# Performance work log

Hardware: AMD Instinct MI355X
Metric: run time of the kernel (lower is better)

## Reference

```python
import jax, jax.numpy as jnp
import numpy as np

B, N, K = 16, 2500, 16
NIN, NMED, WIN, WMED, NETYPE = 64, 64, 32, 32, 3


def _p(key, shape, scale=0.05):
    return jax.random.normal(key, shape, dtype=jnp.float32) * scale


def conv_bn_relu(x, W, b, scale, shift):
    # 1x1 Conv2d (NCHW) + eval-mode BatchNorm folded to affine (scale/shift) + ReLU
    y = jnp.einsum('oc,bcnk->bonk', W, x) + b[None, :, None, None]
    y = y * scale[None, :, None, None] + shift[None, :, None, None]
    return jax.nn.relu(y)


def mp_conv_v2(nf, wf, nn_idx, etype, theta, theta_b, gateW, gate_b, edgeW, edge_b):
    # nf: [B,Cn,N,1], wf: [B,Cw,N,K], nn_idx/etype: [B,N,K]
    n3 = nf[:, :, :, 0]                                   # [B,Cn,N]
    nb = jax.vmap(lambda f, idx: f[:, idx])(n3, nn_idx)   # gather -> [B,Cn,N,K]
    # per-edge-type linear transform of gathered neighbor features (small fixed loop over types)
    msg = jnp.zeros(nb.shape, nb.dtype)
    for t in range(theta.shape[0]):
        mask = (etype == t).astype(nb.dtype)[:, None]     # [B,1,N,K]
        m = jnp.einsum('oi,bink->bonk', theta[t], nb) + theta_b[t][None, :, None, None]
        msg = msg + mask * m
    # edge-feature gate on messages
    gate = jax.nn.sigmoid(jnp.einsum('oc,bcnk->bonk', gateW, wf) + gate_b[None, :, None, None])
    n_out = jax.nn.relu(jnp.mean(msg * gate, axis=3, keepdims=True))  # [B,Cn,N,1]
    # edge update from own feature + gathered neighbor feature
    cat = jnp.concatenate([wf, nb], axis=1)               # [B,Cw+Cn,N,K]
    w_out = jax.nn.relu(jnp.einsum('oc,bcnk->bonk', edgeW, cat) + edge_b[None, :, None, None])
    return n_out, w_out


def setup_inputs() -> dict:
    key = jax.random.key(0)
    ks = jax.random.split(key, 30)
    inp = {
        'node_feature': jax.random.normal(ks[0], (B, NIN, N, 1), jnp.float32),
        'weight_feature': jax.random.normal(ks[1], (B, WIN, N, K), jnp.float32),
        'etype': jax.random.randint(ks[2], (B, N, K), 0, NETYPE, dtype=jnp.int32),
        'nn_idx': jax.random.randint(ks[3], (B, N, K), 0, N, dtype=jnp.int32),
        # nconv1: nin->nmed (conv W,b + folded-BN scale,shift)
        'nW1': _p(ks[4], (NMED, NIN)), 'nb1': _p(ks[5], (NMED,)),
        'ns1': 1.0 + _p(ks[6], (NMED,)), 'nsh1': _p(ks[7], (NMED,)),
        'wW1': _p(ks[8], (WMED, WIN)), 'wb1': _p(ks[9], (WMED,)),
        'ws1': 1.0 + _p(ks[10], (WMED,)), 'wsh1': _p(ks[11], (WMED,)),
        # mp_conv_v2 params
        'theta': _p(ks[12], (NETYPE, NMED, NMED)), 'theta_b': _p(ks[13], (NETYPE, NMED)),
        'gateW': _p(ks[14], (NMED, WMED)), 'gate_b': _p(ks[15], (NMED,)),
        'edgeW': _p(ks[16], (WMED, WMED + NMED)), 'edge_b': _p(ks[17], (WMED,)),
        # nconv2: nmed->nin
        'nW2': _p(ks[18], (NIN, NMED)), 'nb2': _p(ks[19], (NIN,)),
        'ns2': 1.0 + _p(ks[20], (NIN,)), 'nsh2': _p(ks[21], (NIN,)),
        'wW2': _p(ks[22], (WIN, WMED)), 'wb2': _p(ks[23], (WIN,)),
        'ws2': 1.0 + _p(ks[24], (WIN,)), 'wsh2': _p(ks[25], (WIN,)),
    }
    return inp


def reference(node_feature, weight_feature, etype, nn_idx,
              nW1, nb1, ns1, nsh1, wW1, wb1, ws1, wsh1,
              theta, theta_b, gateW, gate_b, edgeW, edge_b,
              nW2, nb2, ns2, nsh2, wW2, wb2, ws2, wsh2):
    nf = conv_bn_relu(node_feature, nW1, nb1, ns1, nsh1)
    wf = conv_bn_relu(weight_feature, wW1, wb1, ws1, wsh1)
    nf, wf = mp_conv_v2(nf, wf, nn_idx, etype, theta, theta_b, gateW, gate_b, edgeW, edge_b)
    nf = conv_bn_relu(nf, nW2, nb2, ns2, nsh2)
    wf = conv_bn_relu(wf, wW2, wb2, ws2, wsh2)
    nf = nf + node_feature   # with_residual=True
    wf = wf + weight_feature
    return (nf, wf)
```

## Files before the change

kernel.cpp:

```cpp
#include <hip/hip_runtime.h>
#include <hip/hip_bf16.h>
#include <stdint.h>

#define B_ 16
#define N_ 2500

typedef unsigned short u16;
typedef __attribute__((ext_vector_type(8))) short bf16x8;
typedef __attribute__((ext_vector_type(4))) float f32x4;

__device__ __forceinline__ u16 f2bf_sw(float f) {
  unsigned u = __float_as_uint(f);
  return (u16)((u + 0x7fffu + ((u >> 16) & 1u)) >> 16);
}
__device__ __forceinline__ u16 f2bf(float f) {
  __hip_bfloat16 h = __float2bfloat16(f);
  return __builtin_bit_cast(u16, h);
}
__device__ __forceinline__ unsigned f2bf2(float lo, float hi) {
  return (unsigned)f2bf(lo) | ((unsigned)f2bf(hi) << 16);
}
__device__ __forceinline__ float sigm(float x) {
  return __builtin_amdgcn_rcpf(1.f + __expf(-x));
}

#define BLOB_U32 12448

__global__ __launch_bounds__(256) void k_pack(
    const float* __restrict__ theta, const float* __restrict__ edgeW,
    const float* __restrict__ gateW, const float* __restrict__ wW1,
    const float* __restrict__ wW2, const float* __restrict__ nW2,
    const float* __restrict__ theta_b, const float* __restrict__ gate_b,
    const float* __restrict__ edge_b,
    const float* __restrict__ ws1, const float* __restrict__ wb1, const float* __restrict__ wsh1,
    const float* __restrict__ ns2, const float* __restrict__ nb2, const float* __restrict__ nsh2,
    const float* __restrict__ ws2, const float* __restrict__ wb2, const float* __restrict__ wsh2,
    unsigned* __restrict__ blob) {
  const int tid = threadIdx.x;
  for (int q = tid; q < 6144; q += 256) {
    int f = q >> 8, lane = (q >> 2) & 63, jp = q & 3;
    int t = f >> 3, mt = (f >> 1) & 3, h = f & 1;
    int el = lane & 15, kg = lane >> 4;
    const float* s = theta + ((size_t)t * 64 + mt * 16 + el) * 64 + h * 32 + kg * 8 + jp * 2;
    blob[q] = (unsigned)f2bf_sw(s[0]) | ((unsigned)f2bf_sw(s[1]) << 16);
  }
  for (int q = tid; q < 1536; q += 256) {
    int f = q >> 8, lane = (q >> 2) & 63, jp = q & 3;
    int mt = f / 3, ss = f - mt * 3;
    int el = lane & 15, kg = lane >> 4;
    const float* s = edgeW + ((size_t)mt * 16 + el) * 96 + ss * 32 + kg * 8 + jp * 2;
    blob[6144 + q] = (unsigned)f2bf_sw(s[0]) | ((unsigned)f2bf_sw(s[1]) << 16);
  }
  for (int q = tid; q < 1024; q += 256) {
    int f = q >> 8, lane = (q >> 2) & 63, jp = q & 3;
    int el = lane & 15, kg = lane >> 4;
    const float* s = gateW + ((size_t)f * 16 + el) * 32 + kg * 8 + jp * 2;
    blob[7680 + q] = (unsigned)f2bf_sw(s[0]) | ((unsigned)f2bf_sw(s[1]) << 16);
  }
  for (int q = tid; q < 512; q += 256) {
    int f = q >> 8, lane = (q >> 2) & 63, jp = q & 3;
    int el = lane & 15, kg = lane >> 4;
    const float* s1 = wW1 + (size_t)(f * 16 + el) * 32 + kg * 8 + jp * 2;
    const float* s2 = wW2 + (size_t)(f * 16 + el) * 32 + kg * 8 + jp * 2;
    blob[8704 + q] = (unsigned)f2bf_sw(s1[0]) | ((unsigned)f2bf_sw(s1[1]) << 16);
    blob[9216 + q] = (unsigned)f2bf_sw(s2[0]) | ((unsigned)f2bf_sw(s2[1]) << 16);
  }
  for (int q = tid; q < 2048; q += 256) {
    int f = q >> 8, lane = (q >> 2) & 63, jp = q & 3;
    int mt = f >> 1, h = f & 1;
    int el = lane & 15, kg = lane >> 4;
    const float* s = nW2 + (size_t)(mt * 16 + el) * 64 + h * 32 + kg * 8 + jp * 2;
    blob[9728 + q] = (unsigned)f2bf_sw(s[0]) | ((unsigned)f2bf_sw(s[1]) << 16);
  }
  float* bf = (float*)blob;
  for (int i = tid; i < 672; i += 256) {
    float v;
    if (i < 192)      v = theta_b[i];
    else if (i < 256) v = gate_b[i - 192];
    else if (i < 320) v = ns2[i - 256];
    else if (i < 384) v = nb2[i - 320];
    else if (i < 448) v = nsh2[i - 384];
    else if (i < 480) v = edge_b[i - 448];
    else if (i < 512) v = ws1[i - 480];
    else if (i < 544) v = wb1[i - 512];
    else if (i < 576) v = wsh1[i - 544];
    else if (i < 608) v = ws2[i - 576];
    else if (i < 640) v = wb2[i - 608];
    else              v = wsh2[i - 640];
    bf[11776 + i] = v;
  }
}

__global__ __launch_bounds__(256) void k_nf1(
    const float* __restrict__ node, const float* __restrict__ W,
    const float* __restrict__ bia, const float* __restrict__ sc,
    const float* __restrict__ sh, u16* __restrict__ nf1b) {
  __shared__ __align__(16) u16 W_p[8 * 64 * 8];
  __shared__ float bia_s[64], sc_s[64], sh_s[64];
  const int tid = threadIdx.x;
  for (int q = tid; q < 2048; q += 256) {
    int f = q >> 8, lane = (q >> 2) & 63, jp = q & 3;
    int mt = f >> 1, h = f & 1;
    int fel = lane & 15, fkg = lane >> 4;
    const float* src = W + (size_t)(mt * 16 + fel) * 64 + h * 32 + fkg * 8 + jp * 2;
    ((unsigned*)W_p)[q] = f2bf2(src[0], src[1]);
  }
  if (tid < 64) { bia_s[tid] = bia[tid]; sc_s[tid] = sc[tid]; sh_s[tid] = sh[tid]; }
  __syncthreads();

  const int l = tid & 63, wv = tid >> 6;
  const int el = l & 15, kg = l >> 4;
  const int bn = blockIdx.x * 64 + wv * 16 + el;
  const int b = bn / N_;
  const int n = bn - b * N_;

  union UF { bf16x8 v; uint4 q; } xb0, xb1;
  const float* xp0 = node + (size_t)(b * 64 + kg * 8) * N_ + n;
  const float* xp1 = node + (size_t)(b * 64 + 32 + kg * 8) * N_ + n;
  {
    float a0[8], a1[8];
#pragma unroll
    for (int j = 0; j < 8; ++j) { a0[j] = xp0[(size_t)j * N_]; a1[j] = xp1[(size_t)j * N_]; }
    xb0.q.x = f2bf2(a0[0], a0[1]); xb0.q.y = f2bf2(a0[2], a0[3]);
    xb0.q.z = f2bf2(a0[4], a0[5]); xb0.q.w = f2bf2(a0[6], a0[7]);
    xb1.q.x = f2bf2(a1[0], a1[1]); xb1.q.y = f2bf2(a1[2], a1[3]);
    xb1.q.z = f2bf2(a1[4], a1[5]); xb1.q.w = f2bf2(a1[6], a1[7]);
  }
  const f32x4 z4 = {0.f, 0.f, 0.f, 0.f};
#pragma unroll
  for (int mt = 0; mt < 4; ++mt) {
    bf16x8 a0 = *(const bf16x8*)&W_p[((mt * 2 + 0) * 64 + l) * 8];
    bf16x8 a1 = *(const bf16x8*)&W_p[((mt * 2 + 1) * 64 + l) * 8];
    f32x4 acc = __builtin_amdgcn_mfma_f32_16x16x32_bf16(a0, xb0.v, z4, 0, 0, 0);
    acc = __builtin_amdgcn_mfma_f32_16x16x32_bf16(a1, xb1.v, acc, 0, 0, 0);
    int ob = mt * 16 + kg * 4;
    float4 s4 = *(const float4*)&sc_s[ob];
    float4 b4 = *(const float4*)&bia_s[ob];
    float4 h4 = *(const float4*)&sh_s[ob];
    uint2 d;
    d.x = f2bf2(fmaxf(fmaf(s4.x, acc[0] + b4.x, h4.x), 0.f),
                fmaxf(fmaf(s4.y, acc[1] + b4.y, h4.y), 0.f));
    d.y = f2bf2(fmaxf(fmaf(s4.z, acc[2] + b4.z, h4.z), 0.f),
                fmaxf(fmaf(s4.w, acc[3] + b4.w, h4.w), 0.f));
    *(uint2*)&nf1b[(size_t)bn * 64 + ob] = d;
  }
}

__global__ __launch_bounds__(512, 2) void k_fused(
    const float* __restrict__ node, const float* __restrict__ wfeat,
    const int* __restrict__ etype, const int* __restrict__ nn_idx,
    const u16* __restrict__ nf1b, const unsigned* __restrict__ blob,
    float* __restrict__ out_nf, float* __restrict__ out_wf) {

  __shared__ __align__(16) unsigned char sm[BLOB_U32 * 4];
  __shared__ __align__(16) u16 nout_bf[32 * 64];
  __shared__ __align__(16) u16 Rx[8][512];

  const int tid = threadIdx.x;
  for (int i = tid; i < BLOB_U32 / 4; i += 512)
    ((uint4*)sm)[i] = ((const uint4*)blob)[i];

  const u16* th_p   = (const u16*)sm;
  const u16* eW_p   = (const u16*)(sm + 24576);
  const u16* gW_p   = (const u16*)(sm + 30720);
  const u16* w1_p   = (const u16*)(sm + 34816);
  const u16* w2_p   = (const u16*)(sm + 36864);
  const u16* nW2f_p = (const u16*)(sm + 38912);
  const float* par = (const float*)(sm + 47104);
  const float* tb_s  = par;
  const float* gb_s  = par + 192;
  const float* ns2_s = par + 256;
  const float* nb2_s = par + 320;
  const float* nsh2_s= par + 384;
  const float* eb_s  = par + 448;
  const float* ws1_s = par + 480;
  const float* wb1_s = par + 512;
  const float* wsh1_s= par + 544;
  const float* ws2_s = par + 576;
  const float* wb2_s = par + 608;
  const float* wsh2_s= par + 640;

  const int pb = blockIdx.x;
  const int xcd = pb & 7, sub = pb >> 3;
  const int lb = (xcd < 2) ? (xcd * 157 + sub) : (2 * 157 + (xcd - 2) * 156 + sub);
  const int nbase = lb * 32;

  const int l = tid & 63, wv = tid >> 6;
  const int el = l & 15, kg = l >> 4;
  u16* const Rn = &Rx[wv][0];

  __syncthreads();

  const f32x4 z4 = {0.f, 0.f, 0.f, 0.f};

  int idxv[4], etv[4];
  bf16x8 nb0v[4], nb1v[4];
  union UF { bf16x8 v; uint4 q; } xv[4];

  idxv[0] = nn_idx[(nbase + wv) * 16 + el];
  etv[0]  = etype[(nbase + wv) * 16 + el];
  idxv[1] = nn_idx[(nbase + 8 + wv) * 16 + el];
  etv[1]  = etype[(nbase + 8 + wv) * 16 + el];
  {
    const int nid = nbase + wv;
    const int b = nid / N_, n = nid - b * N_;
    const u16* nbp = nf1b + ((size_t)b * N_ + idxv[0]) * 64 + kg * 8;
    nb0v[0] = *(const bf16x8*)nbp;
    nb1v[0] = *(const bf16x8*)(nbp + 32);
    const float* xp = wfeat + ((size_t)(b * 32 + kg * 8) * N_ + n) * 16 + el;
    float a[8];
#pragma unroll
    for (int j = 0; j < 8; ++j) a[j] = xp[(size_t)j * N_ * 16];
    xv[0].q.x = f2bf2(a[0], a[1]); xv[0].q.y = f2bf2(a[2], a[3]);
    xv[0].q.z = f2bf2(a[4], a[5]); xv[0].q.w = f2bf2(a[6], a[7]);
  }

#pragma unroll
  for (int it = 0; it < 4; ++it) {
    const int nid = nbase + it * 8 + wv;
    const int b = nid / N_;
    const int n = nid - b * N_;
    const int nl = it * 8 + wv;
    const int et = etv[it];

    if (it + 2 < 4) {
      idxv[it + 2] = nn_idx[(nbase + (it + 2) * 8 + wv) * 16 + el];
      etv[it + 2]  = etype[(nbase + (it + 2) * 8 + wv) * 16 + el];
    }
    if (it + 1 < 4) {
      const int nid2 = nbase + (it + 1) * 8 + wv;
      const int b2 = nid2 / N_, n2 = nid2 - b2 * N_;
      const u16* nbp = nf1b + ((size_t)b2 * N_ + idxv[it + 1]) * 64 + kg * 8;
      nb0v[it + 1] = *(const bf16x8*)nbp;
      nb1v[it + 1] = *(const bf16x8*)(nbp + 32);
      const float* xp = wfeat + ((size_t)(b2 * 32 + kg * 8) * N_ + n2) * 16 + el;
      float a[8];
#pragma unroll
      for (int j = 0; j < 8; ++j) a[j] = xp[(size_t)j * N_ * 16];
      xv[it + 1].q.x = f2bf2(a[0], a[1]); xv[it + 1].q.y = f2bf2(a[2], a[3]);
      xv[it + 1].q.z = f2bf2(a[4], a[5]); xv[it + 1].q.w = f2bf2(a[6], a[7]);
    }

#pragma unroll
    for (int mt = 0; mt < 2; ++mt) {
      bf16x8 a = *(const bf16x8*)&w1_p[(mt * 64 + l) * 8];
      f32x4 wc = __builtin_amdgcn_mfma_f32_16x16x32_bf16(a, xv[it].v, z4, 0, 0, 0);
      int ob = mt * 16 + kg * 4;
      float4 s4 = *(const float4*)&ws1_s[ob];
      float4 b4 = *(const float4*)&wb1_s[ob];
      float4 h4 = *(const float4*)&wsh1_s[ob];
      uint2 d;
      d.x = f2bf2(fmaxf(fmaf(s4.x, wc[0] + b4.x, h4.x), 0.f),
                  fmaxf(fmaf(s4.y, wc[1] + b4.y, h4.y), 0.f));
      d.y = f2bf2(fmaxf(fmaf(s4.z, wc[2] + b4.z, h4.z), 0.f),
                  fmaxf(fmaf(s4.w, wc[3] + b4.w, h4.w), 0.f));
      *(uint2*)&Rn[((mt * 2 + (kg >> 1)) * 16 + el) * 8 + (kg & 1) * 4] = d;
    }
    bf16x8 wff = *(const bf16x8*)&Rn[l * 8];

    f32x4 macc[4] = {z4, z4, z4, z4};
    {
      union { bf16x8 v; uint4 q; } nb0u, nb1u;
      nb0u.v = nb0v[it]; nb1u.v = nb1v[it];
#pragma unroll
      for (int t = 0; t < 3; ++t) {
        unsigned msk = (et == t) ? 0xffffffffu : 0u;
        union { bf16x8 v; uint4 q; } b0, b1;
        b0.q.x = nb0u.q.x & msk; b0.q.y = nb0u.q.y & msk;
        b0.q.z = nb0u.q.z & msk; b0.q.w = nb0u.q.w & msk;
        b1.q.x = nb1u.q.x & msk; b1.q.y = nb1u.q.y & msk;
        b1.q.z = nb1u.q.z & msk; b1.q.w = nb1u.q.w & msk;
#pragma unroll
        for (int mt = 0; mt < 4; ++mt) {
          bf16x8 a0 = *(const bf16x8*)&th_p[((t * 8 + mt * 2 + 0) * 64 + l) * 8];
          bf16x8 a1 = *(const bf16x8*)&th_p[((t * 8 + mt * 2 + 1) * 64 + l) * 8];
          macc[mt] = __builtin_amdgcn_mfma_f32_16x16x32_bf16(a0, b0.v, macc[mt], 0, 0, 0);
          macc[mt] = __builtin_amdgcn_mfma_f32_16x16x32_bf16(a1, b1.v, macc[mt], 0, 0, 0);
        }
      }
    }

    f32x4 eacc[2];
#pragma unroll
    for (int mt = 0; mt < 2; ++mt) {
      bf16x8 a0 = *(const bf16x8*)&eW_p[((mt * 3 + 0) * 64 + l) * 8];
      bf16x8 a1 = *(const bf16x8*)&eW_p[((mt * 3 + 1) * 64 + l) * 8];
      bf16x8 a2 = *(const bf16x8*)&eW_p[((mt * 3 + 2) * 64 + l) * 8];
      f32x4 acc = __builtin_amdgcn_mfma_f32_16x16x32_bf16(a0, wff, z4, 0, 0, 0);
      acc = __builtin_amdgcn_mfma_f32_16x16x32_bf16(a1, nb0v[it], acc, 0, 0, 0);
      acc = __builtin_amdgcn_mfma_f32_16x16x32_bf16(a2, nb1v[it], acc, 0, 0, 0);
      eacc[mt] = acc;
    }

    float p[16];
#pragma unroll
    for (int mt = 0; mt < 4; ++mt) {
      bf16x8 ga = *(const bf16x8*)&gW_p[(mt * 64 + l) * 8];
      f32x4 g = __builtin_amdgcn_mfma_f32_16x16x32_bf16(ga, wff, z4, 0, 0, 0);
      int ob = mt * 16 + kg * 4;
      float4 tb = *(const float4*)&tb_s[et * 64 + ob];
      float4 gb = *(const float4*)&gb_s[ob];
      p[mt * 4 + 0] = (macc[mt][0] + tb.x) * sigm(g[0] + gb.x);
      p[mt * 4 + 1] = (macc[mt][1] + tb.y) * sigm(g[1] + gb.y);
      p[mt * 4 + 2] = (macc[mt][2] + tb.z) * sigm(g[2] + gb.z);
      p[mt * 4 + 3] = (macc[mt][3] + tb.w) * sigm(g[3] + gb.w);
    }

    {
      const int b0 = el & 1, b1 = (el >> 1) & 1, b2 = (el >> 2) & 1, b3 = (el >> 3) & 1;
      float w8[8];
#pragma unroll
      for (int j = 0; j < 8; ++j) {
        float send = b0 ? p[2 * j] : p[2 * j + 1];
        float keep = b0 ? p[2 * j + 1] : p[2 * j];
        w8[j] = keep + __shfl_xor(send, 1);
      }
      float w4[4];
#pragma unroll
      for (int j = 0; j < 4; ++j) {
        float send = b1 ? w8[2 * j] : w8[2 * j + 1];
        float keep = b1 ? w8[2 * j + 1] : w8[2 * j];
        w4[j] = keep + __shfl_xor(send, 2);
      }
      float w2[2];
#pragma unroll
      for (int j = 0; j < 2; ++j) {
        float send = b2 ? w4[2 * j] : w4[2 * j + 1];
        float keep = b2 ? w4[2 * j + 1] : w4[2 * j];
        w2[j] = keep + __shfl_xor(send, 4);
      }
      float send = b3 ? w2[0] : w2[1];
      float keep = b3 ? w2[1] : w2[0];
      float z = keep + __shfl_xor(send, 8);
      float no = fmaxf(z * 0.0625f, 0.f);
      int ch = ((el >> 2) << 4) + (kg << 2) + (el & 3);
      int su = (ch >> 3) ^ (nl & 7);
      nout_bf[nl * 64 + su * 8 + (ch & 7)] = f2bf(no);
    }

#pragma unroll
    for (int mt = 0; mt < 2; ++mt) {
      int ob = mt * 16 + kg * 4;
      float4 eb4 = *(const float4*)&eb_s[ob];
      uint2 d;
      d.x = f2bf2(fmaxf(eacc[mt][0] + eb4.x, 0.f), fmaxf(eacc[mt][1] + eb4.y, 0.f));
      d.y = f2bf2(fmaxf(eacc[mt][2] + eb4.z, 0.f), fmaxf(eacc[mt][3] + eb4.w, 0.f));
      *(uint2*)&Rn[((mt * 2 + (kg >> 1)) * 16 + el) * 8 + (kg & 1) * 4] = d;
    }
    bf16x8 wof = *(const bf16x8*)&Rn[l * 8];

#pragma unroll
    for (int mt = 0; mt < 2; ++mt) {
      bf16x8 a = *(const bf16x8*)&w2_p[(mt * 64 + l) * 8];
      f32x4 fc = __builtin_amdgcn_mfma_f32_16x16x32_bf16(a, wof, z4, 0, 0, 0);
      int ob = mt * 16 + kg * 4;
      float4 s4 = *(const float4*)&ws2_s[ob];
      float4 b4 = *(const float4*)&wb2_s[ob];
      float4 h4 = *(const float4*)&wsh2_s[ob];
      float sv[4] = {s4.x, s4.y, s4.z, s4.w};
      float bv[4] = {b4.x, b4.y, b4.z, b4.w};
      float hv[4] = {h4.x, h4.y, h4.z, h4.w};
#pragma unroll
      for (int r = 0; r < 4; ++r) {
        int a2 = ((b * 32 + ob + r) * N_ + n) * 16 + el;
        float y = fmaxf(fmaf(sv[r], fc[r] + bv[r], hv[r]), 0.f);
        out_wf[a2] = y + wfeat[a2];
      }
    }
  }
  __syncthreads();

  {
    const int mt = wv & 3, ng = wv >> 2;
    const int node_l = ng * 16 + el;
    const int nid2 = nbase + node_l;
    const int b2 = nid2 / N_;
    const int n2 = nid2 - b2 * N_;
    const int sw = node_l & 7;
    bf16x8 nb0 = *(const bf16x8*)&nout_bf[node_l * 64 + ((0 + kg) ^ sw) * 8];
    bf16x8 nb1 = *(const bf16x8*)&nout_bf[node_l * 64 + ((4 + kg) ^ sw) * 8];
    bf16x8 a0 = *(const bf16x8*)&nW2f_p[((mt * 2 + 0) * 64 + l) * 8];
    bf16x8 a1 = *(const bf16x8*)&nW2f_p[((mt * 2 + 1) * 64 + l) * 8];
    f32x4 acc = __builtin_amdgcn_mfma_f32_16x16x32_bf16(a0, nb0, z4, 0, 0, 0);
    acc = __builtin_amdgcn_mfma_f32_16x16x32_bf16(a1, nb1, acc, 0, 0, 0);
#pragma unroll
    for (int i = 0; i < 4; ++i) {
      int ch = mt * 16 + kg * 4 + i;
      int off = (b2 * 64 + ch) * N_ + n2;
      float y = fmaxf(fmaf(ns2_s[ch], acc[i] + nb2_s[ch], nsh2_s[ch]), 0.f);
      out_nf[off] = y + node[off];
    }
  }
}

extern "C" void kernel_launch(void* const* d_in, const int* in_sizes, int n_in,
                              void* d_out, int out_size, void* d_ws, size_t ws_size,
                              hipStream_t stream) {
  const float* node    = (const float*)d_in[0];
  const float* wfeat   = (const float*)d_in[1];
  const int*   etype   = (const int*)d_in[2];
  const int*   nn_idx  = (const int*)d_in[3];
  const float* nW1     = (const float*)d_in[4];
  const float* nb1     = (const float*)d_in[5];
  const float* ns1     = (const float*)d_in[6];
  const float* nsh1    = (const float*)d_in[7];
  const float* wW1     = (const float*)d_in[8];
  const float* wb1     = (const float*)d_in[9];
  const float* ws1     = (const float*)d_in[10];
  const float* wsh1    = (const float*)d_in[11];
  const float* theta   = (const float*)d_in[12];
  const float* theta_b = (const float*)d_in[13];
  const float* gateW   = (const float*)d_in[14];
  const float* gate_b  = (const float*)d_in[15];
  const float* edgeW   = (const float*)d_in[16];
  const float* edge_b  = (const float*)d_in[17];
  const float* nW2     = (const float*)d_in[18];
  const float* nb2     = (const float*)d_in[19];
  const float* ns2     = (const float*)d_in[20];
  const float* nsh2    = (const float*)d_in[21];
  const float* wW2     = (const float*)d_in[22];
  const float* wb2     = (const float*)d_in[23];
  const float* ws2     = (const float*)d_in[24];
  const float* wsh2    = (const float*)d_in[25];

  u16*      nf1b = (u16*)d_ws;
  unsigned* blob = (unsigned*)((char*)d_ws + 5120000);
  float* out_nf = (float*)d_out;
  float* out_wf = (float*)d_out + (size_t)B_ * 64 * N_;

  k_pack<<<1, 256, 0, stream>>>(theta, edgeW, gateW, wW1, wW2, nW2,
                                theta_b, gate_b, edge_b,
                                ws1, wb1, wsh1, ns2, nb2, nsh2, ws2, wb2, wsh2,
                                blob);
  k_nf1<<<625, 256, 0, stream>>>(node, nW1, nb1, ns1, nsh1, nf1b);
  k_fused<<<1250, 512, 0, stream>>>(node, wfeat, etype, nn_idx, nf1b, blob,
                                    out_nf, out_wf);
}
```

Measured before the change: 129.3 us.

## Switch fused edge kernel from 16x16x32 to 32x32x16 MFMA tiles

Repacks all weight fragments in the pack kernel for the 32x32x16 bf16 MFMA layout and restructures the fused kernel so each wave handles two nodes (32 edges) per iteration over two iterations instead of one node over four. This cuts the MFMA instruction count, reuses each weight operand across more columns, and halves the loop trip count. In exchange it uses larger f32x16 accumulators, which raises register pressure under the 512-thread, 2-block launch bound, and doubles the per-wave LDS staging buffer. The mean reduction shuffle tree is extended to 32 values per lane.

```diff
diff --git a/kernel.cpp b/kernel.cpp
--- a/kernel.cpp
+++ b/kernel.cpp
@@ -8,6 +8,7 @@
 typedef unsigned short u16;
 typedef __attribute__((ext_vector_type(8))) short bf16x8;
 typedef __attribute__((ext_vector_type(4))) float f32x4;
+typedef __attribute__((ext_vector_type(16))) float f32x16;
 
 __device__ __forceinline__ u16 f2bf_sw(float f) {
   unsigned u = __float_as_uint(f);
@@ -39,29 +40,29 @@
   const int tid = threadIdx.x;
   for (int q = tid; q < 6144; q += 256) {
     int f = q >> 8, lane = (q >> 2) & 63, jp = q & 3;
-    int t = f >> 3, mt = (f >> 1) & 3, h = f & 1;
-    int el = lane & 15, kg = lane >> 4;
-    const float* s = theta + ((size_t)t * 64 + mt * 16 + el) * 64 + h * 32 + kg * 8 + jp * 2;
-    blob[q] = (unsigned)f2bf_sw(s[0]) | ((unsigned)f2bf_sw(s[1]) << 16);
+    int t = f >> 3, mt = (f >> 2) & 1, s = f & 3;
+    int m = lane & 31, hf = lane >> 5;
+    const float* src = theta + ((size_t)t * 64 + mt * 32 + m) * 64 + s * 16 + hf * 8 + jp * 2;
+    blob[q] = (unsigned)f2bf_sw(src[0]) | ((unsigned)f2bf_sw(src[1]) << 16);
   }
   for (int q = tid; q < 1536; q += 256) {
     int f = q >> 8, lane = (q >> 2) & 63, jp = q & 3;
-    int mt = f / 3, ss = f - mt * 3;
-    int el = lane & 15, kg = lane >> 4;
-    const float* s = edgeW + ((size_t)mt * 16 + el) * 96 + ss * 32 + kg * 8 + jp * 2;
-    blob[6144 + q] = (unsigned)f2bf_sw(s[0]) | ((unsigned)f2bf_sw(s[1]) << 16);
+    int m = lane & 31, hf = lane >> 5;
+    const float* src = edgeW + (size_t)m * 96 + f * 16 + hf * 8 + jp * 2;
+    blob[6144 + q] = (unsigned)f2bf_sw(src[0]) | ((unsigned)f2bf_sw(src[1]) << 16);
   }
   for (int q = tid; q < 1024; q += 256) {
     int f = q >> 8, lane = (q >> 2) & 63, jp = q & 3;
-    int el = lane & 15, kg = lane >> 4;
-    const float* s = gateW + ((size_t)f * 16 + el) * 32 + kg * 8 + jp * 2;
-    blob[7680 + q] = (unsigned)f2bf_sw(s[0]) | ((unsigned)f2bf_sw(s[1]) << 16);
+    int mt = f >> 1, s = f & 1;
+    int m = lane & 31, hf = lane >> 5;
+    const float* src = gateW + ((size_t)mt * 32 + m) * 32 + s * 16 + hf * 8 + jp * 2;
+    blob[7680 + q] = (unsigned)f2bf_sw(src[0]) | ((unsigned)f2bf_sw(src[1]) << 16);
   }
   for (int q = tid; q < 512; q += 256) {
     int f = q >> 8, lane = (q >> 2) & 63, jp = q & 3;
-    int el = lane & 15, kg = lane >> 4;
-    const float* s1 = wW1 + (size_t)(f * 16 + el) * 32 + kg * 8 + jp * 2;
-    const float* s2 = wW2 + (size_t)(f * 16 + el) * 32 + kg * 8 + jp * 2;
+    int m = lane & 31, hf = lane >> 5;
+    const float* s1 = wW1 + (size_t)m * 32 + f * 16 + hf * 8 + jp * 2;
+    const float* s2 = wW2 + (size_t)m * 32 + f * 16 + hf * 8 + jp * 2;
     blob[8704 + q] = (unsigned)f2bf_sw(s1[0]) | ((unsigned)f2bf_sw(s1[1]) << 16);
     blob[9216 + q] = (unsigned)f2bf_sw(s2[0]) | ((unsigned)f2bf_sw(s2[1]) << 16);
   }
@@ -154,7 +155,7 @@
 
   __shared__ __align__(16) unsigned char sm[BLOB_U32 * 4];
   __shared__ __align__(16) u16 nout_bf[32 * 64];
-  __shared__ __align__(16) u16 Rx[8][512];
+  __shared__ __align__(16) u16 Rx[8][1024];
 
   const int tid = threadIdx.x;
   for (int i = tid; i < BLOB_U32 / 4; i += 512)
@@ -186,197 +187,239 @@
   const int nbase = lb * 32;
 
   const int l = tid & 63, wv = tid >> 6;
-  const int el = l & 15, kg = l >> 4;
-  u16* const Rn = &Rx[wv][0];
+  const int col = l & 31, half = l >> 5;
+  const int en = col & 15, nd = col >> 4;
+  u16* const Rw = &Rx[wv][0];
 
   __syncthreads();
 
-  const f32x4 z4 = {0.f, 0.f, 0.f, 0.f};
-
-  int idxv[4], etv[4];
-  bf16x8 nb0v[4], nb1v[4];
-  union UF { bf16x8 v; uint4 q; } xv[4];
-
-  idxv[0] = nn_idx[(nbase + wv) * 16 + el];
-  etv[0]  = etype[(nbase + wv) * 16 + el];
-  idxv[1] = nn_idx[(nbase + 8 + wv) * 16 + el];
-  etv[1]  = etype[(nbase + 8 + wv) * 16 + el];
+  const f32x16 z16 = {0.f,0.f,0.f,0.f,0.f,0.f,0.f,0.f,0.f,0.f,0.f,0.f,0.f,0.f,0.f,0.f};
+
+  int idxv[2], etv[2];
+  bf16x8 nbf[2][4];
+  bf16x8 xf[2][2];
+
+  idxv[0] = nn_idx[(nbase + 2 * wv + nd) * 16 + en];
+  etv[0]  = etype[(nbase + 2 * wv + nd) * 16 + en];
+  idxv[1] = nn_idx[(nbase + 16 + 2 * wv + nd) * 16 + en];
+  etv[1]  = etype[(nbase + 16 + 2 * wv + nd) * 16 + en];
   {
-    const int nid = nbase + wv;
+    const int nid = nbase + 2 * wv + nd;
     const int b = nid / N_, n = nid - b * N_;
-    const u16* nbp = nf1b + ((size_t)b * N_ + idxv[0]) * 64 + kg * 8;
-    nb0v[0] = *(const bf16x8*)nbp;
-    nb1v[0] = *(const bf16x8*)(nbp + 32);
-    const float* xp = wfeat + ((size_t)(b * 32 + kg * 8) * N_ + n) * 16 + el;
-    float a[8];
-#pragma unroll
-    for (int j = 0; j < 8; ++j) a[j] = xp[(size_t)j * N_ * 16];
-    xv[0].q.x = f2bf2(a[0], a[1]); xv[0].q.y = f2bf2(a[2], a[3]);
-    xv[0].q.z = f2bf2(a[4], a[5]); xv[0].q.w = f2bf2(a[6], a[7]);
-  }
-
-#pragma unroll
-  for (int it = 0; it < 4; ++it) {
-    const int nid = nbase + it * 8 + wv;
+    const u16* nbp = nf1b + ((size_t)b * N_ + idxv[0]) * 64 + half * 8;
+#pragma unroll
+    for (int s = 0; s < 4; ++s) nbf[0][s] = *(const bf16x8*)(nbp + s * 16);
+    const float* xpp = wfeat + ((size_t)(b * 32 + half * 8) * N_ + n) * 16 + en;
+#pragma unroll
+    for (int s = 0; s < 2; ++s) {
+      float a[8];
+#pragma unroll
+      for (int j = 0; j < 8; ++j) a[j] = xpp[(size_t)(s * 16 + j) * N_ * 16];
+      union { bf16x8 v; uint4 q; } u;
+      u.q.x = f2bf2(a[0], a[1]); u.q.y = f2bf2(a[2], a[3]);
+      u.q.z = f2bf2(a[4], a[5]); u.q.w = f2bf2(a[6], a[7]);
+      xf[0][s] = u.v;
+    }
+  }
+
+#pragma unroll
+  for (int it = 0; it < 2; ++it) {
+    const int nid = nbase + it * 16 + 2 * wv + nd;
     const int b = nid / N_;
     const int n = nid - b * N_;
-    const int nl = it * 8 + wv;
+    const int nl = it * 16 + 2 * wv + nd;
     const int et = etv[it];
 
-    if (it + 2 < 4) {
-      idxv[it + 2] = nn_idx[(nbase + (it + 2) * 8 + wv) * 16 + el];
-      etv[it + 2]  = etype[(nbase + (it + 2) * 8 + wv) * 16 + el];
-    }
-    if (it + 1 < 4) {
-      const int nid2 = nbase + (it + 1) * 8 + wv;
+    if (it == 0) {
+      const int nid2 = nbase + 16 + 2 * wv + nd;
       const int b2 = nid2 / N_, n2 = nid2 - b2 * N_;
-      const u16* nbp = nf1b + ((size_t)b2 * N_ + idxv[it + 1]) * 64 + kg * 8;
-      nb0v[it + 1] = *(const bf16x8*)nbp;
-      nb1v[it + 1] = *(const bf16x8*)(nbp + 32);
-      const float* xp = wfeat + ((size_t)(b2 * 32 + kg * 8) * N_ + n2) * 16 + el;
-      float a[8];
-#pragma unroll
-      for (int j = 0; j < 8; ++j) a[j] = xp[(size_t)j * N_ * 16];
-      xv[it + 1].q.x = f2bf2(a[0], a[1]); xv[it + 1].q.y = f2bf2(a[2], a[3]);
-      xv[it + 1].q.z = f2bf2(a[4], a[5]); xv[it + 1].q.w = f2bf2(a[6], a[7]);
-    }
-
+      const u16* nbp = nf1b + ((size_t)b2 * N_ + idxv[1]) * 64 + half * 8;
+#pragma unroll
+      for (int s = 0; s < 4; ++s) nbf[1][s] = *(const bf16x8*)(nbp + s * 16);
+      const float* xpp = wfeat + ((size_t)(b2 * 32 + half * 8) * N_ + n2) * 16 + en;
+#pragma unroll
+      for (int s = 0; s < 2; ++s) {
+        float a[8];
+#pragma unroll
+        for (int j = 0; j < 8; ++j) a[j] = xpp[(size_t)(s * 16 + j) * N_ * 16];
+        union { bf16x8 v; uint4 q; } u;
+        u.q.x = f2bf2(a[0], a[1]); u.q.y = f2bf2(a[2], a[3]);
+        u.q.z = f2bf2(a[4], a[5]); u.q.w = f2bf2(a[6], a[7]);
+        xf[1][s] = u.v;
+      }
+    }
+
+    f32x16 wc;
+    {
+      bf16x8 a0 = *(const bf16x8*)&w1_p[(0 * 64 + l) * 8];
+      bf16x8 a1 = *(const bf16x8*)&w1_p[(1 * 64 + l) * 8];
+      wc = __builtin_amdgcn_mfma_f32_32x32x16_bf16(a0, xf[it][0], z16, 0, 0, 0);
+      wc = __builtin_amdgcn_mfma_f32_32x32x16_bf16(a1, xf[it][1], wc, 0, 0, 0);
+    }
+#pragma unroll
+    for (int q = 0; q < 4; ++q) {
+      int chb = q * 8 + 4 * half;
+      float4 s4 = *(const float4*)&ws1_s[chb];
+      float4 b4 = *(const float4*)&wb1_s[chb];
+      float4 h4 = *(const float4*)&wsh1_s[chb];
+      float y0 = fmaxf(fmaf(s4.x, wc[q * 4 + 0] + b4.x, h4.x), 0.f);
+      float y1 = fmaxf(fmaf(s4.y, wc[q * 4 + 1] + b4.y, h4.y), 0.f);
+      float y2 = fmaxf(fmaf(s4.z, wc[q * 4 + 2] + b4.z, h4.z), 0.f);
+      float y3 = fmaxf(fmaf(s4.w, wc[q * 4 + 3] + b4.w, h4.w), 0.f);
+      uint2 d; d.x = f2bf2(y0, y1); d.y = f2bf2(y2, y3);
+      int Q = 2 * q + half;
+      *(uint2*)&Rw[(Q >> 2) * 512 + (col + 32 * ((Q >> 1) & 1)) * 8 + (Q & 1) * 4] = d;
+    }
+    bf16x8 wff0 = *(const bf16x8*)&Rw[l * 8];
+    bf16x8 wff1 = *(const bf16x8*)&Rw[512 + l * 8];
+
+    f32x16 eacc;
+    {
+      bf16x8 e0 = *(const bf16x8*)&eW_p[(0 * 64 + l) * 8];
+      bf16x8 e1 = *(const bf16x8*)&eW_p[(1 * 64 + l) * 8];
+      bf16x8 e2 = *(const bf16x8*)&eW_p[(2 * 64 + l) * 8];
+      bf16x8 e3 = *(const bf16x8*)&eW_p[(3 * 64 + l) * 8];
+      bf16x8 e4 = *(const bf16x8*)&eW_p[(4 * 64 + l) * 8];
+      bf16x8 e5 = *(const bf16x8*)&eW_p[(5 * 64 + l) * 8];
+      eacc = __builtin_amdgcn_mfma_f32_32x32x16_bf16(e0, wff0, z16, 0, 0, 0);
+      eacc = __builtin_amdgcn_mfma_f32_32x32x16_bf16(e1, wff1, eacc, 0, 0, 0);
+      eacc = __builtin_amdgcn_mfma_f32_32x32x16_bf16(e2, nbf[it][0], eacc, 0, 0, 0);
+      eacc = __builtin_amdgcn_mfma_f32_32x32x16_bf16(e3, nbf[it][1], eacc, 0, 0, 0);
+      eacc = __builtin_amdgcn_mfma_f32_32x32x16_bf16(e4, nbf[it][2], eacc, 0, 0, 0);
+      eacc = __builtin_amdgcn_mfma_f32_32x32x16_bf16(e5, nbf[it][3], eacc, 0, 0, 0);
+    }
+#pragma unroll
+    for (int q = 0; q < 4; ++q) {
+      int chb = q * 8 + 4 * half;
+      float4 eb4 = *(const float4*)&eb_s[chb];
+      float y0 = fmaxf(eacc[q * 4 + 0] + eb4.x, 0.f);
+      float y1 = fmaxf(eacc[q * 4 + 1] + eb4.y, 0.f);
+      float y2 = fmaxf(eacc[q * 4 + 2] + eb4.z, 0.f);
+      float y3 = fmaxf(eacc[q * 4 + 3] + eb4.w, 0.f);
+      uint2 d; d.x = f2bf2(y0, y1); d.y = f2bf2(y2, y3);
+      int Q = 2 * q + half;
+      *(uint2*)&Rw[(Q >> 2) * 512 + (col + 32 * ((Q >> 1) & 1)) * 8 + (Q & 1) * 4] = d;
+    }
+    bf16x8 wof0 = *(const bf16x8*)&Rw[l * 8];
+    bf16x8 wof1 = *(const bf16x8*)&Rw[512 + l * 8];
+
+    f32x16 macc0 = z16, macc1 = z16;
+#pragma unroll
+    for (int t = 0; t < 3; ++t) {
+      unsigned msk = (et == t) ? 0xffffffffu : 0u;
+      bf16x8 bm[4];
+#pragma unroll
+      for (int s = 0; s < 4; ++s) {
+        union { bf16x8 v; uint4 q; } u;
+        u.v = nbf[it][s];
+        u.q.x &= msk; u.q.y &= msk; u.q.z &= msk; u.q.w &= msk;
+        bm[s] = u.v;
+      }
+#pragma unroll
+      for (int s = 0; s < 4; ++s) {
+        bf16x8 a0 = *(const bf16x8*)&th_p[((t * 8 + 0 * 4 + s) * 64 + l) * 8];
+        bf16x8 a1 = *(const bf16x8*)&th_p[((t * 8 + 1 * 4 + s) * 64 + l) * 8];
+        macc0 = __builtin_amdgcn_mfma_f32_32x32x16_bf16(a0, bm[s], macc0, 0, 0, 0);
+        macc1 = __builtin_amdgcn_mfma_f32_32x32x16_bf16(a1, bm[s], macc1, 0, 0, 0);
+      }
+    }
+
+    float p[32];
 #pragma unroll
     for (int mt = 0; mt < 2; ++mt) {
-      bf16x8 a = *(const bf16x8*)&w1_p[(mt * 64 + l) * 8];
-      f32x4 wc = __builtin_amdgcn_mfma_f32_16x16x32_bf16(a, xv[it].v, z4, 0, 0, 0);
-      int ob = mt * 16 + kg * 4;
-      float4 s4 = *(const float4*)&ws1_s[ob];
-      float4 b4 = *(const float4*)&wb1_s[ob];
-      float4 h4 = *(const float4*)&wsh1_s[ob];
-      uint2 d;
-      d.x = f2bf2(fmaxf(fmaf(s4.x, wc[0] + b4.x, h4.x), 0.f),
-                  fmaxf(fmaf(s4.y, wc[1] + b4.y, h4.y), 0.f));
-      d.y = f2bf2(fmaxf(fmaf(s4.z, wc[2] + b4.z, h4.z), 0.f),
-                  fmaxf(fmaf(s4.w, wc[3] + b4.w, h4.w), 0.f));
-      *(uint2*)&Rn[((mt * 2 + (kg >> 1)) * 16 + el) * 8 + (kg & 1) * 4] = d;
-    }
-    bf16x8 wff = *(const bf16x8*)&Rn[l * 8];
-
-    f32x4 macc[4] = {z4, z4, z4, z4};
+      bf16x8 g0 = *(const bf16x8*)&gW_p[((mt * 2 + 0) * 64 + l) * 8];
+      bf16x8 g1 = *(const bf16x8*)&gW_p[((mt * 2 + 1) * 64 + l) * 8];
+      f32x16 gacc = __builtin_amdgcn_mfma_f32_32x32x16_bf16(g0, wff0, z16, 0, 0, 0);
+      gacc = __builtin_amdgcn_mfma_f32_32x32x16_bf16(g1, wff1, gacc, 0, 0, 0);
+#pragma unroll
+      for (int q = 0; q < 4; ++q) {
+        int chb = mt * 32 + q * 8 + 4 * half;
+        float4 tb4 = *(const float4*)&tb_s[et * 64 + chb];
+        float4 gb4 = *(const float4*)&gb_s[chb];
+        float mv0 = (mt ? macc1[q * 4 + 0] : macc0[q * 4 + 0]) + tb4.x;
+        float mv1 = (mt ? macc1[q * 4 + 1] : macc0[q * 4 + 1]) + tb4.y;
+        float mv2 = (mt ? macc1[q * 4 + 2] : macc0[q * 4 + 2]) + tb4.z;
+        float mv3 = (mt ? macc1[q * 4 + 3] : macc0[q * 4 + 3]) + tb4.w;
+        p[mt * 16 + q * 4 + 0] = mv0 * sigm(gacc[q * 4 + 0] + gb4.x);
+        p[mt * 16 + q * 4 + 1] = mv1 * sigm(gacc[q * 4 + 1] + gb4.y);
+        p[mt * 16 + q * 4 + 2] = mv2 * sigm(gacc[q * 4 + 2] + gb4.z);
+        p[mt * 16 + q * 4 + 3] = mv3 * sigm(gacc[q * 4 + 3] + gb4.w);
+      }
+    }
+
     {
-      union { bf16x8 v; uint4 q; } nb0u, nb1u;
-      nb0u.v = nb0v[it]; nb1u.v = nb1v[it];
-#pragma unroll
-      for (int t = 0; t < 3; ++t) {
-        unsigned msk = (et == t) ? 0xffffffffu : 0u;
-        union { bf16x8 v; uint4 q; } b0, b1;
-        b0.q.x = nb0u.q.x & msk; b0.q.y = nb0u.q.y & msk;
-        b0.q.z = nb0u.q.z & msk; b0.q.w = nb0u.q.w & msk;
-        b1.q.x = nb1u.q.x & msk; b1.q.y = nb1u.q.y & msk;
-        b1.q.z = nb1u.q.z & msk; b1.q.w = nb1u.q.w & msk;
-#pragma unroll
-        for (int mt = 0; mt < 4; ++mt) {
-          bf16x8 a0 = *(const bf16x8*)&th_p[((t * 8 + mt * 2 + 0) * 64 + l) * 8];
-          bf16x8 a1 = *(const bf16x8*)&th_p[((t * 8 + mt * 2 + 1) * 64 + l) * 8];
-          macc[mt] = __builtin_amdgcn_mfma_f32_16x16x32_bf16(a0, b0.v, macc[mt], 0, 0, 0);
-          macc[mt] = __builtin_amdgcn_mfma_f32_16x16x32_bf16(a1, b1.v, macc[mt], 0, 0, 0);
-        }
-      }
-    }
-
-    f32x4 eacc[2];
-#pragma unroll
-    for (int mt = 0; mt < 2; ++mt) {
-      bf16x8 a0 = *(const bf16x8*)&eW_p[((mt * 3 + 0) * 64 + l) * 8];
-      bf16x8 a1 = *(const bf16x8*)&eW_p[((mt * 3 + 1) * 64 + l) * 8];
-      bf16x8 a2 = *(const bf16x8*)&eW_p[((mt * 3 + 2) * 64 + l) * 8];
-      f32x4 acc = __builtin_amdgcn_mfma_f32_16x16x32_bf16(a0, wff, z4, 0, 0, 0);
-      acc = __builtin_amdgcn_mfma_f32_16x16x32_bf16(a1, nb0v[it], acc, 0, 0, 0);
-      acc = __builtin_amdgcn_mfma_f32_16x16x32_bf16(a2, nb1v[it], acc, 0, 0, 0);
-      eacc[mt] = acc;
-    }
-
-    float p[16];
-#pragma unroll
-    for (int mt = 0; mt < 4; ++mt) {
-      bf16x8 ga = *(const bf16x8*)&gW_p[(mt * 64 + l) * 8];
-      f32x4 g = __builtin_amdgcn_mfma_f32_16x16x32_bf16(ga, wff, z4, 0, 0, 0);
-      int ob = mt * 16 + kg * 4;
-      float4 tb = *(const float4*)&tb_s[et * 64 + ob];
-      float4 gb = *(const float4*)&gb_s[ob];
-      p[mt * 4 + 0] = (macc[mt][0] + tb.x) * sigm(g[0] + gb.x);
-      p[mt * 4 + 1] = (macc[mt][1] + tb.y) * sigm(g[1] + gb.y);
-      p[mt * 4 + 2] = (macc[mt][2] + tb.z) * sigm(g[2] + gb.z);
-      p[mt * 4 + 3] = (macc[mt][3] + tb.w) * sigm(g[3] + gb.w);
-    }
-
-    {
-      const int b0 = el & 1, b1 = (el >> 1) & 1, b2 = (el >> 2) & 1, b3 = (el >> 3) & 1;
-      float w8[8];
-#pragma unroll
-      for (int j = 0; j < 8; ++j) {
+      const int b0 = en & 1, b1 = (en >> 1) & 1, b2 = (en >> 2) & 1, b3 = (en >> 3) & 1;
+      float r16[16];
+#pragma unroll
+      for (int j = 0; j < 16; ++j) {
         float send = b0 ? p[2 * j] : p[2 * j + 1];
         float keep = b0 ? p[2 * j + 1] : p[2 * j];
-        w8[j] = keep + __shfl_xor(send, 1);
-      }
-      float w4[4];
+        r16[j] = keep + __shfl_xor(send, 1);
+      }
+      float r8[8];
+#pragma unroll
+      for (int j = 0; j < 8; ++j) {
+        float send = b1 ? r16[2 * j] : r16[2 * j + 1];
+        float keep = b1 ? r16[2 * j + 1] : r16[2 * j];
+        r8[j] = keep + __shfl_xor(send, 2);
+      }
+      float r4[4];
 #pragma unroll
       for (int j = 0; j < 4; ++j) {
-        float send = b1 ? w8[2 * j] : w8[2 * j + 1];
-        float keep = b1 ? w8[2 * j + 1] : w8[2 * j];
-        w4[j] = keep + __shfl_xor(send, 2);
-      }
-      float w2[2];
+        float send = b2 ? r8[2 * j] : r8[2 * j + 1];
+        float keep = b2 ? r8[2 * j + 1] : r8[2 * j];
+        r4[j] = keep + __shfl_xor(send, 4);
+      }
+      float r2[2];
 #pragma unroll
       for (int j = 0; j < 2; ++j) {
-        float send = b2 ? w4[2 * j] : w4[2 * j + 1];
-        float keep = b2 ? w4[2 * j + 1] : w4[2 * j];
-        w2[j] = keep + __shfl_xor(send, 4);
-      }
-      float send = b3 ? w2[0] : w2[1];
-      float keep = b3 ? w2[1] : w2[0];
-      float z = keep + __shfl_xor(send, 8);
-      float no = fmaxf(z * 0.0625f, 0.f);
-      int ch = ((el >> 2) << 4) + (kg << 2) + (el & 3);
-      int su = (ch >> 3) ^ (nl & 7);
-      nout_bf[nl * 64 + su * 8 + (ch & 7)] = f2bf(no);
-    }
-
-#pragma unroll
-    for (int mt = 0; mt < 2; ++mt) {
-      int ob = mt * 16 + kg * 4;
-      float4 eb4 = *(const float4*)&eb_s[ob];
-      uint2 d;
-      d.x = f2bf2(fmaxf(eacc[mt][0] + eb4.x, 0.f), fmaxf(eacc[mt][1] + eb4.y, 0.f));
-      d.y = f2bf2(fmaxf(eacc[mt][2] + eb4.z, 0.f), fmaxf(eacc[mt][3] + eb4.w, 0.f));
-      *(uint2*)&Rn[((mt * 2 + (kg >> 1)) * 16 + el) * 8 + (kg & 1) * 4] = d;
-    }
-    bf16x8 wof = *(const bf16x8*)&Rn[l * 8];
-
-#pragma unroll
-    for (int mt = 0; mt < 2; ++mt) {
-      bf16x8 a = *(const bf16x8*)&w2_p[(mt * 64 + l) * 8];
-      f32x4 fc = __builtin_amdgcn_mfma_f32_16x16x32_bf16(a, wof, z4, 0, 0, 0);
-      int ob = mt * 16 + kg * 4;
-      float4 s4 = *(const float4*)&ws2_s[ob];
-      float4 b4 = *(const float4*)&wb2_s[ob];
-      float4 h4 = *(const float4*)&wsh2_s[ob];
-      float sv[4] = {s4.x, s4.y, s4.z, s4.w};
-      float bv[4] = {b4.x, b4.y, b4.z, b4.w};
-      float hv[4] = {h4.x, h4.y, h4.z, h4.w};
-#pragma unroll
-      for (int r = 0; r < 4; ++r) {
-        int a2 = ((b * 32 + ob + r) * N_ + n) * 16 + el;
-        float y = fmaxf(fmaf(sv[r], fc[r] + bv[r], hv[r]), 0.f);
-        out_wf[a2] = y + wfeat[a2];
+        float send = b3 ? r4[2 * j] : r4[2 * j + 1];
+        float keep = b3 ? r4[2 * j + 1] : r4[2 * j];
+        r2[j] = keep + __shfl_xor(send, 8);
+      }
+      int ch0 = (en & 3) + 8 * ((en >> 2) & 3) + 4 * half;
+      float v0 = fmaxf(r2[0] * 0.0625f, 0.f);
+      float v1 = fmaxf(r2[1] * 0.0625f, 0.f);
+      nout_bf[nl * 64 + (((ch0 >> 3) ^ (nl & 7)) << 3) + (ch0 & 7)] = f2bf(v0);
+      int ch1 = ch0 + 32;
+      nout_bf[nl * 64 + (((ch1 >> 3) ^ (nl & 7)) << 3) + (ch1 & 7)] = f2bf(v1);
+    }
+
+    {
+      bf16x8 a0 = *(const bf16x8*)&w2_p[(0 * 64 + l) * 8];
+      bf16x8 a1 = *(const bf16x8*)&w2_p[(1 * 64 + l) * 8];
+      f32x16 fc = __builtin_amdgcn_mfma_f32_32x32x16_bf16(a0, wof0, z16, 0, 0, 0);
+      fc = __builtin_amdgcn_mfma_f32_32x32x16_bf16(a1, wof1, fc, 0, 0, 0);
+#pragma unroll
+      for (int q = 0; q < 4; ++q) {
+        int chb = q * 8 + 4 * half;
+        float4 s4 = *(const float4*)&ws2_s[chb];
+        float4 b4 = *(const float4*)&wb2_s[chb];
+        float4 h4 = *(const float4*)&wsh2_s[chb];
+        float sv[4] = {s4.x, s4.y, s4.z, s4.w};
+        float bv[4] = {b4.x, b4.y, b4.z, b4.w};
+        float hv[4] = {h4.x, h4.y, h4.z, h4.w};
+#pragma unroll
+        for (int i = 0; i < 4; ++i) {
+          int ch = chb + i;
+          size_t a2 = (((size_t)b * 32 + ch) * N_ + n) * 16 + en;
+          float y = fmaxf(fmaf(sv[i], fc[q * 4 + i] + bv[i], hv[i]), 0.f);
+          out_wf[a2] = y + wfeat[a2];
+        }
       }
     }
   }
   __syncthreads();
 
   {
+    const int el = l & 15, kg = l >> 4;
     const int mt = wv & 3, ng = wv >> 2;
     const int node_l = ng * 16 + el;
     const int nid2 = nbase + node_l;
     const int b2 = nid2 / N_;
     const int n2 = nid2 - b2 * N_;
     const int sw = node_l & 7;
+    const f32x4 z4 = {0.f, 0.f, 0.f, 0.f};
     bf16x8 nb0 = *(const bf16x8*)&nout_bf[node_l * 64 + ((0 + kg) ^ sw) * 8];
     bf16x8 nb1 = *(const bf16x8*)&nout_bf[node_l * 64 + ((4 + kg) ^ sw) * 8];
     bf16x8 a0 = *(const bf16x8*)&nW2f_p[((mt * 2 + 0) * 64 + l) * 8];
@@ -386,7 +429,7 @@
 #pragma unroll
     for (int i = 0; i < 4; ++i) {
       int ch = mt * 16 + kg * 4 + i;
-      int off = (b2 * 64 + ch) * N_ + n2;
+      size_t off = ((size_t)b2 * 64 + ch) * N_ + n2;
       float y = fmaxf(fmaf(ns2_s[ch], acc[i] + nb2_s[ch], nsh2_s[ch]), 0.f);
       out_nf[off] = y + node[off];
     }
```

New measurement: 132.8 us. +2.7%, slower.

## Drop software prefetch pipeline and raise occupancy to four blocks per CU

Applied to the files above, without the earlier changes.

Removes the register-held prefetch of neighbor features, edge types and weight features for the next iterations, and instead loads each iteration's data just before use inside a non-unrolled loop. Launch bounds go from 2 to 4 blocks of 512 threads per CU, so the kernel must fit in far fewer VGPRs. The aim is to hide gather latency through more resident waves rather than explicit prefetch. The risks are exposed load latency within each wave and possible spills under the tighter register budget. LDS use per block (a weight blob plus staging buffers) may also cap how many blocks actually fit.

```diff
diff --git a/kernel.cpp b/kernel.cpp
--- a/kernel.cpp
+++ b/kernel.cpp
@@ -146,7 +146,7 @@
   }
 }
 
-__global__ __launch_bounds__(512, 2) void k_fused(
+__global__ __launch_bounds__(512, 4) void k_fused(
     const float* __restrict__ node, const float* __restrict__ wfeat,
     const int* __restrict__ etype, const int* __restrict__ nn_idx,
     const u16* __restrict__ nf1b, const unsigned* __restrict__ blob,
@@ -193,58 +193,35 @@
 
   const f32x4 z4 = {0.f, 0.f, 0.f, 0.f};
 
-  int idxv[4], etv[4];
-  bf16x8 nb0v[4], nb1v[4];
-  union UF { bf16x8 v; uint4 q; } xv[4];
-
-  idxv[0] = nn_idx[(nbase + wv) * 16 + el];
-  etv[0]  = etype[(nbase + wv) * 16 + el];
-  idxv[1] = nn_idx[(nbase + 8 + wv) * 16 + el];
-  etv[1]  = etype[(nbase + 8 + wv) * 16 + el];
-  {
-    const int nid = nbase + wv;
-    const int b = nid / N_, n = nid - b * N_;
-    const u16* nbp = nf1b + ((size_t)b * N_ + idxv[0]) * 64 + kg * 8;
-    nb0v[0] = *(const bf16x8*)nbp;
-    nb1v[0] = *(const bf16x8*)(nbp + 32);
-    const float* xp = wfeat + ((size_t)(b * 32 + kg * 8) * N_ + n) * 16 + el;
-    float a[8];
-#pragma unroll
-    for (int j = 0; j < 8; ++j) a[j] = xp[(size_t)j * N_ * 16];
-    xv[0].q.x = f2bf2(a[0], a[1]); xv[0].q.y = f2bf2(a[2], a[3]);
-    xv[0].q.z = f2bf2(a[4], a[5]); xv[0].q.w = f2bf2(a[6], a[7]);
-  }
-
-#pragma unroll
+#pragma unroll 1
   for (int it = 0; it < 4; ++it) {
     const int nid = nbase + it * 8 + wv;
     const int b = nid / N_;
     const int n = nid - b * N_;
     const int nl = it * 8 + wv;
-    const int et = etv[it];
-
-    if (it + 2 < 4) {
-      idxv[it + 2] = nn_idx[(nbase + (it + 2) * 8 + wv) * 16 + el];
-      etv[it + 2]  = etype[(nbase + (it + 2) * 8 + wv) * 16 + el];
-    }
-    if (it + 1 < 4) {
-      const int nid2 = nbase + (it + 1) * 8 + wv;
-      const int b2 = nid2 / N_, n2 = nid2 - b2 * N_;
-      const u16* nbp = nf1b + ((size_t)b2 * N_ + idxv[it + 1]) * 64 + kg * 8;
-      nb0v[it + 1] = *(const bf16x8*)nbp;
-      nb1v[it + 1] = *(const bf16x8*)(nbp + 32);
-      const float* xp = wfeat + ((size_t)(b2 * 32 + kg * 8) * N_ + n2) * 16 + el;
+    const int ebase = nid * 16;
+
+    const int idx = nn_idx[ebase + el];
+    const int et  = etype[ebase + el];
+
+    const u16* nbp = nf1b + ((size_t)b * N_ + idx) * 64 + kg * 8;
+    bf16x8 nbf0 = *(const bf16x8*)nbp;
+    bf16x8 nbf1 = *(const bf16x8*)(nbp + 32);
+
+    union UF { bf16x8 v; uint4 q; } xf;
+    {
+      const float* xp = wfeat + ((size_t)(b * 32 + kg * 8) * N_ + n) * 16 + el;
       float a[8];
 #pragma unroll
       for (int j = 0; j < 8; ++j) a[j] = xp[(size_t)j * N_ * 16];
-      xv[it + 1].q.x = f2bf2(a[0], a[1]); xv[it + 1].q.y = f2bf2(a[2], a[3]);
-      xv[it + 1].q.z = f2bf2(a[4], a[5]); xv[it + 1].q.w = f2bf2(a[6], a[7]);
+      xf.q.x = f2bf2(a[0], a[1]); xf.q.y = f2bf2(a[2], a[3]);
+      xf.q.z = f2bf2(a[4], a[5]); xf.q.w = f2bf2(a[6], a[7]);
     }
 
 #pragma unroll
     for (int mt = 0; mt < 2; ++mt) {
       bf16x8 a = *(const bf16x8*)&w1_p[(mt * 64 + l) * 8];
-      f32x4 wc = __builtin_amdgcn_mfma_f32_16x16x32_bf16(a, xv[it].v, z4, 0, 0, 0);
+      f32x4 wc = __builtin_amdgcn_mfma_f32_16x16x32_bf16(a, xf.v, z4, 0, 0, 0);
       int ob = mt * 16 + kg * 4;
       float4 s4 = *(const float4*)&ws1_s[ob];
       float4 b4 = *(const float4*)&wb1_s[ob];
@@ -261,7 +238,7 @@
     f32x4 macc[4] = {z4, z4, z4, z4};
     {
       union { bf16x8 v; uint4 q; } nb0u, nb1u;
-      nb0u.v = nb0v[it]; nb1u.v = nb1v[it];
+      nb0u.v = nbf0; nb1u.v = nbf1;
 #pragma unroll
       for (int t = 0; t < 3; ++t) {
         unsigned msk = (et == t) ? 0xffffffffu : 0u;
@@ -287,8 +264,8 @@
       bf16x8 a1 = *(const bf16x8*)&eW_p[((mt * 3 + 1) * 64 + l) * 8];
       bf16x8 a2 = *(const bf16x8*)&eW_p[((mt * 3 + 2) * 64 + l) * 8];
       f32x4 acc = __builtin_amdgcn_mfma_f32_16x16x32_bf16(a0, wff, z4, 0, 0, 0);
-      acc = __builtin_amdgcn_mfma_f32_16x16x32_bf16(a1, nb0v[it], acc, 0, 0, 0);
-      acc = __builtin_amdgcn_mfma_f32_16x16x32_bf16(a2, nb1v[it], acc, 0, 0, 0);
+      acc = __builtin_amdgcn_mfma_f32_16x16x32_bf16(a1, nbf0, acc, 0, 0, 0);
+      acc = __builtin_amdgcn_mfma_f32_16x16x32_bf16(a2, nbf1, acc, 0, 0, 0);
       eacc[mt] = acc;
     }
 
```

New measurement: 409.4 us. 3.17x slower.
